# Performance work log

Hardware: AMD Instinct MI355X
Metric: run time of the kernel (lower is better)

## Reference

```python
import jax, jax.numpy as jnp
import numpy as np
from jax import lax

B, T_MEL, M = 4, 63, 80
HOP, K_UP, WIN = 256, 800, 1024
R, S, Q = 120, 240, 256
NB, K, CYCLE = 16, 2, 8
PAD_UP = (K_UP + 4 * HOP - WIN) // 2  # 400
L = (T_MEL - 1) * HOP  # 15872


def conv1d(x, w, b, dilation=1, pad=(0, 0)):
    # x: [B,Cin,L], w: [Cout,Cin,K]
    y = lax.conv_general_dilated(x, w, (1,), [pad], rhs_dilation=(dilation,),
                                 dimension_numbers=('NCH', 'OIH', 'NCH'))
    return y + b[None, :, None]


def setup_inputs() -> dict:
    key = jax.random.key(0)
    ks = jax.random.split(key, 20)
    rn = lambda k, shape, s=0.05: (jax.random.normal(k, shape, jnp.float32) * s)
    return {
        'waveforms': jax.random.normal(ks[0], (B, L), jnp.float32),
        'melspecs': jax.random.normal(ks[1], (B, M, T_MEL), jnp.float32),
        # ConvTranspose1d weight, torch layout (in, out, k)
        'w_up': rn(ks[2], (M, M, K_UP)), 'b_up': rn(ks[3], (M,)),
        'w_in': rn(ks[4], (R, 1, 1)), 'b_in': rn(ks[5], (R,)),
        # per-block params stacked on leading axis
        'w_gate': rn(ks[6], (NB, 2 * R, R, K)), 'b_gate': rn(ks[7], (NB, 2 * R)),
        'w_cond': rn(ks[8], (NB, 2 * R, M, 1)), 'b_cond': rn(ks[9], (NB, 2 * R)),
        'w_res': rn(ks[10], (NB, R, R, 1)), 'b_res': rn(ks[11], (NB, R)),
        'w_skip': rn(ks[12], (NB, S, R, 1)), 'b_skip': rn(ks[13], (NB, S)),
        'w_h1': rn(ks[14], (Q, S, 1)), 'b_h1': rn(ks[15], (Q,)),
        'w_h2': rn(ks[16], (Q, Q, 1)), 'b_h2': rn(ks[17], (Q,)),
    }


def reference(waveforms, melspecs, w_up, b_up, w_in, b_in, w_gate, b_gate,
              w_cond, b_cond, w_res, b_res, w_skip, b_skip, w_h1, b_h1, w_h2, b_h2):
    # upsample = ConvTranspose1d: lhs-dilated conv with flipped, transposed kernel
    wt = jnp.flip(jnp.transpose(w_up, (1, 0, 2)), -1)  # [out,in,k]
    p = K_UP - 1 - PAD_UP  # 399
    conditions = lax.conv_general_dilated(
        melspecs, wt, (1,), [(p, p)], lhs_dilation=(HOP,),
        dimension_numbers=('NCH', 'OIH', 'NCH')) + b_up[None, :, None]

    length = min(waveforms.shape[-1], conditions.shape[-1])
    wav = waveforms[..., :length]
    cond = conditions[..., :length]

    residuals = conv1d(wav[:, None, :], w_in, b_in)  # [B,R,L]
    skips = jnp.zeros((wav.shape[0], S, length), residuals.dtype)
    for i in range(NB):
        d = 2 ** (i % CYCLE)
        gated = conv1d(residuals, w_gate[i], b_gate[i], dilation=d, pad=((K - 1) * d, 0))
        gated = gated + conv1d(cond, w_cond[i], b_cond[i])
        f, g = jnp.split(gated, 2, axis=1)
        z = jnp.tanh(f) * jax.nn.sigmoid(g)  # [B,R,L]
        skips = skips + conv1d(z, w_skip[i], b_skip[i])
        residuals = residuals + conv1d(z, w_res[i], b_res[i])

    h = conv1d(jax.nn.relu(skips), w_h1, b_h1)
    logits = conv1d(jax.nn.relu(h), w_h2, b_h2)  # [B,Q,L]
    return logits
```

## Files before the change

kernel.cpp:

```cpp
#include <hip/hip_runtime.h>
#include <math.h>

#define B_   4
#define M_   80
#define TMEL 63
#define R_   120
#define S_   240
#define Q_   256
#define NB_  16
#define L_   15872

typedef float  f32x4  __attribute__((ext_vector_type(4)));
typedef short  bf16x8 __attribute__((ext_vector_type(8)));
typedef short  short4_t __attribute__((ext_vector_type(4)));

__device__ __forceinline__ short f2bf(float x) {
  unsigned u = __builtin_bit_cast(unsigned, x);
  u += 0x7fffu + ((u >> 16) & 1u);
  return (short)(u >> 16);
}
__device__ __forceinline__ float bf2f(unsigned short s) {
  unsigned u = ((unsigned)s) << 16;
  return __builtin_bit_cast(float, u);
}

__global__ __launch_bounds__(256) void prep_melT_kernel(
    const float* __restrict__ mel, short* __restrict__ melT)
{
  const int idx = blockIdx.x * 256 + threadIdx.x;
  if (idx >= B_ * TMEL * M_) return;
  const int m = idx % M_;
  const int i = (idx / M_) % TMEL;
  const int b = idx / (M_ * TMEL);
  melT[idx] = f2bf(mel[b * (M_ * TMEL) + m * TMEL + i]);
}

__global__ __launch_bounds__(256) void prep_wup_kernel(
    const float* __restrict__ w_up, short* __restrict__ Wup)
{
  __shared__ float T[M_][65];
  const int c  = blockIdx.x >> 4;
  const int j  = (blockIdx.x >> 2) & 3;
  const int fb = blockIdx.x & 3;
  for (int idx = threadIdx.x; idx < M_ * 64; idx += 256) {
    const int pl = idx & 63, m = idx >> 6;
    const int phi = fb * 64 + pl;
    const int dmin = (phi < 112) ? -1 : -2;
    const int dmax = (phi < 144) ? 1 : 0;
    const int delta = dmin + j;
    float v = 0.0f;
    if (delta <= dmax)
      v = w_up[m * (M_ * 800) + c * 800 + (400 + phi + 256 * delta)];
    T[m][pl] = v;
  }
  __syncthreads();
  for (int idx = threadIdx.x; idx < 64 * M_; idx += 256) {
    const int m = idx % M_, pl = idx / M_;
    const int phi = fb * 64 + pl;
    Wup[((size_t)phi * M_ + c) * 320 + j * 80 + m] = f2bf(T[m][pl]);
  }
}

#define KPU 328

__global__ __launch_bounds__(256, 2) void upsample_mfma_kernel(
    const short* __restrict__ melT, const short* __restrict__ Wup,
    const float* __restrict__ b_up, short* __restrict__ condb)
{
  __shared__ __align__(16) short Xu[64 * KPU];
  const int tid = threadIdx.x;
  const int phi = blockIdx.x;
  const int r0 = blockIdx.y * 64;
  const int dmin = (phi < 112) ? -1 : -2;

  for (int idx = tid; idx < 2560; idx += 256) {
    const int v = idx % 10;
    const int j = (idx / 10) & 3;
    const int rl = idx / 40;
    const int rho = r0 + rl;
    const int b = rho / 62;
    const int n = rho - b * 62;
    const int i = n - (dmin + j);
    int4 val = make_int4(0, 0, 0, 0);
    if (b < B_ && i >= 0 && i < TMEL)
      val = *(const int4*)&melT[((size_t)b * TMEL + i) * M_ + v * 8];
    *(int4*)&Xu[rl * KPU + j * 80 + v * 8] = val;
  }
  __syncthreads();

  const int lane = tid & 63;
  const int wv = tid >> 6;
  const int col = lane & 15;
  const int quad = lane >> 4;
  const int kq = quad * 8;

  f32x4 acc[5];
#pragma unroll
  for (int i = 0; i < 5; ++i) acc[i] = (f32x4)(0.f);
#pragma unroll
  for (int ks = 0; ks < 10; ++ks) {
    bf16x8 a = *(const bf16x8*)&Xu[(wv * 16 + col) * KPU + ks * 32 + kq];
#pragma unroll
    for (int ct = 0; ct < 5; ++ct) {
      bf16x8 b = *(const bf16x8*)(Wup + ((size_t)phi * M_ + ct * 16 + col) * 320 + ks * 32 + kq);
      acc[ct] = __builtin_amdgcn_mfma_f32_16x16x32_bf16(a, b, acc[ct], 0, 0, 0);
    }
  }
#pragma unroll
  for (int ct = 0; ct < 5; ++ct) {
    const int c = ct * 16 + col;
    const float bc = b_up[c];
#pragma unroll
    for (int reg = 0; reg < 4; ++reg) {
      const int rho = r0 + wv * 16 + quad * 4 + reg;
      if (rho < 248) {
        const int b = rho / 62;
        const int n = rho - b * 62;
        const int t = phi + (n << 8);
        condb[((size_t)b * L_ + t) * M_ + c] = f2bf(acc[ct][reg] + bc);
      }
    }
  }
}

__global__ __launch_bounds__(256) void in_conv_kernel(
    const float* __restrict__ wav, const float* __restrict__ w_in,
    const float* __restrict__ b_in, float* __restrict__ res)
{
  const int idx = blockIdx.x * 256 + threadIdx.x;
  const int r = idx & 127;
  const int rem = idx >> 7;
  const int t = rem % L_;
  const int b = rem / L_;
  res[idx] = (r < R_) ? (w_in[r] * wav[b * L_ + t] + b_in[r]) : 0.0f;
}

__global__ __launch_bounds__(256) void prepack_w1_kernel(
    const float* __restrict__ wg, const float* __restrict__ wc,
    short* __restrict__ W1p)
{
  const int idx = blockIdx.x * 256 + threadIdx.x;
  const int k = idx % 320;
  const int cp = (idx / 320) % 256;
  const int i = idx / (320 * 256);
  float val = 0.0f;
  if (cp < 240) {
    const int r = cp >> 1;
    const int corig = (cp & 1) ? (120 + r) : r;
    if (k < 120)      val = wg[((size_t)(i * 240 + corig) * 120 + k) * 2 + 0];
    else if (k < 240) val = wg[((size_t)(i * 240 + corig) * 120 + (k - 120)) * 2 + 1];
    else              val = wc[(size_t)(i * 240 + corig) * 80 + (k - 240)];
  }
  W1p[idx] = f2bf(val);
}

__global__ __launch_bounds__(256) void prepack_w2_kernel(
    const float* __restrict__ wsk, const float* __restrict__ wr,
    short* __restrict__ W2p)
{
  const int idx = blockIdx.x * 256 + threadIdx.x;
  const int k = idx % 128;
  const int sp = (idx / 128) % 384;
  const int i = idx / (128 * 384);
  float val = 0.0f;
  if (k < 120) {
    if (sp < 240)      val = wsk[(size_t)(i * 240 + sp) * 120 + k];
    else if (sp < 360) val = wr[(size_t)(i * 120 + (sp - 240)) * 120 + k];
  }
  W2p[idx] = f2bf(val);
}

__global__ __launch_bounds__(256) void prepack_rest_kernel(
    const float* __restrict__ wh1, const float* __restrict__ wh2,
    const float* __restrict__ bg, const float* __restrict__ bc,
    const float* __restrict__ bs, const float* __restrict__ br,
    short* __restrict__ Wh1p, short* __restrict__ Wh2p,
    float* __restrict__ bias1p, float* __restrict__ bias2p)
{
  const int idx = blockIdx.x * 256 + threadIdx.x;
  if (idx < 65536) {
    const int q = idx >> 8, k = idx & 255;
    Wh1p[idx] = f2bf(k < 240 ? wh1[q * 240 + k] : 0.0f);
  } else if (idx < 131072) {
    Wh2p[idx - 65536] = f2bf(wh2[idx - 65536]);
  } else if (idx < 134912) {
    const int j = idx - 131072;
    const int i = j / 240, cp = j % 240;
    const int r = cp >> 1;
    const int corig = (cp & 1) ? (120 + r) : r;
    bias1p[j] = bg[i * 240 + corig] + bc[i * 240 + corig];
  } else if (idx < 141056) {
    const int j = idx - 134912;
    const int i = j / 384, sp = j % 384;
    float v = 0.0f;
    if (sp < 240)      v = bs[i * 240 + sp];
    else if (sp < 360) v = br[i * 120 + (sp - 240)];
    bias2p[j] = v;
  }
}

#define KP1 320
#define KP2 136
#define SGP 248
#define NTILE (L_ / 64)
#define NWG   (NTILE * B_)
#define CPX   (NWG / 8)

__device__ __forceinline__ int xswz(int row, int k) {
  return row * KP1 + (k ^ ((row & 7) << 3));
}

__global__ __launch_bounds__(512, 4) void block_mfma_kernel(
    const float* __restrict__ res_in, float* __restrict__ res_out,
    unsigned short* __restrict__ skips, const short* __restrict__ condb,
    const short* __restrict__ W1, const short* __restrict__ W2,
    const float* __restrict__ bias1, const float* __restrict__ bias2,
    const int d, const int first)
{
  __shared__ __align__(16) short Xs[64 * KP1];
  short* const Zs = Xs;

  const int tid = threadIdx.x;
  const int w_id = blockIdx.y * NTILE + blockIdx.x;
  const int nid  = (w_id & 7) * CPX + (w_id >> 3);
  const int bb   = nid / NTILE;
  const int t0   = (nid - bb * NTILE) * 64;

  {
    const int dd = (d <= 64) ? d : 64;
    const int nr = 64 + dd;
    for (int idx = tid; idx < nr * 30; idx += 512) {
      const int rr = idx / 30, c4 = idx - rr * 30;
      int ts;
      if (d <= 64)      ts = t0 - d + rr;
      else              ts = (rr < 64) ? (t0 - 128 + rr) : (t0 + rr - 64);
      float4 v = make_float4(0.f, 0.f, 0.f, 0.f);
      if (ts >= 0)
        v = *(const float4*)(res_in + ((size_t)(bb * L_ + ts) * 128 + c4 * 4));
      short4_t s;
      s.x = f2bf(v.x); s.y = f2bf(v.y); s.z = f2bf(v.z); s.w = f2bf(v.w);
      if (rr < 64)
        *(short4_t*)&Xs[xswz(rr, c4 * 4)] = s;
      const int r1 = rr - dd;
      if (r1 >= 0)
        *(short4_t*)&Xs[xswz(r1, 120 + c4 * 4)] = s;
    }
  }
  for (int idx = tid; idx < 640; idx += 512) {
    const int c = idx % 10, trw = idx / 10;
    const int4 v = *(const int4*)(condb + ((size_t)(bb * L_ + t0 + trw) * M_ + c * 8));
    *(int4*)&Xs[xswz(trw, 240 + c * 8)] = v;
  }
  __syncthreads();

  const int lane = tid & 63;
  const int wv = tid >> 6;
  const int col = lane & 15;
  const int quad = lane >> 4;
  const int kq = quad * 8;

  f32x4 acc[4][2];
#pragma unroll
  for (int a = 0; a < 4; ++a)
#pragma unroll
    for (int b = 0; b < 2; ++b) acc[a][b] = (f32x4)(0.f);
#pragma unroll
  for (int ks = 0; ks < 10; ++ks) {
    bf16x8 av[4];
#pragma unroll
    for (int tf = 0; tf < 4; ++tf)
      av[tf] = *(const bf16x8*)&Xs[xswz(tf * 16 + col, ks * 32 + kq)];
#pragma unroll
    for (int ct = 0; ct < 2; ++ct) {
      bf16x8 b = *(const bf16x8*)(W1 + ((wv * 2 + ct) * 16 + col) * 320 + ks * 32 + kq);
#pragma unroll
      for (int tf = 0; tf < 4; ++tf)
        acc[tf][ct] = __builtin_amdgcn_mfma_f32_16x16x32_bf16(av[tf], b, acc[tf][ct], 0, 0, 0);
    }
  }

  __syncthreads();

#pragma unroll
  for (int ct = 0; ct < 2; ++ct) {
    const int tile = wv * 2 + ct;
    if (tile < 15) {
      const int cp = tile * 16 + col;
      const float bias = bias1[cp];
#pragma unroll
      for (int tf = 0; tf < 4; ++tf) {
#pragma unroll
        for (int reg = 0; reg < 4; ++reg) {
          float v = acc[tf][ct][reg] + bias;
          v = fminf(fmaxf(v, -15.f), 15.f);
          const float e = __expf((lane & 1) ? -v : 2.0f * v);
          const float rc = __builtin_amdgcn_rcpf(e + 1.0f);
          const float u = (lane & 1) ? rc : (e - 1.0f) * rc;
          const float p = __shfl_xor(u, 1, 64);
          if (!(lane & 1)) {
            const int t = tf * 16 + quad * 4 + reg;
            Zs[t * KP2 + tile * 8 + (col >> 1)] = f2bf(u * p);
          }
        }
      }
    }
  }
  if (tid < 64)
    *(int4*)&Zs[tid * KP2 + 120] = make_int4(0, 0, 0, 0);
  __syncthreads();

  f32x4 acc2[4][3];
#pragma unroll
  for (int a = 0; a < 4; ++a)
#pragma unroll
    for (int b = 0; b < 3; ++b) acc2[a][b] = (f32x4)(0.f);
#pragma unroll
  for (int ks = 0; ks < 4; ++ks) {
    bf16x8 av[4];
#pragma unroll
    for (int tf = 0; tf < 4; ++tf)
      av[tf] = *(const bf16x8*)&Zs[(tf * 16 + col) * KP2 + ks * 32 + kq];
#pragma unroll
    for (int st = 0; st < 3; ++st) {
      bf16x8 b = *(const bf16x8*)(W2 + ((wv * 3 + st) * 16 + col) * 128 + ks * 32 + kq);
#pragma unroll
      for (int tf = 0; tf < 4; ++tf)
        acc2[tf][st] = __builtin_amdgcn_mfma_f32_16x16x32_bf16(av[tf], b, acc2[tf][st], 0, 0, 0);
    }
  }

  __syncthreads();

  short* SG = Xs;
#pragma unroll
  for (int st = 0; st < 3; ++st) {
    const int tile = wv * 3 + st;
    if (tile < 15) {
      const int s = tile * 16 + col;
      const float b2 = bias2[s];
#pragma unroll
      for (int tf = 0; tf < 4; ++tf)
#pragma unroll
        for (int reg = 0; reg < 4; ++reg)
          SG[(tf * 16 + quad * 4 + reg) * SGP + s] = f2bf(acc2[tf][st][reg] + b2);
    } else if (tile < 23) {
      const int s = tile * 16 + col;
      const int r = s - 240;
      if (r < 120) {
        const float b2 = bias2[s];
#pragma unroll
        for (int tf = 0; tf < 4; ++tf) {
#pragma unroll
          for (int reg = 0; reg < 4; ++reg) {
            const int t = tf * 16 + quad * 4 + reg;
            const size_t gi = ((size_t)(bb * L_ + t0 + t)) * 128 + r;
            res_out[gi] = res_in[gi] + acc2[tf][st][reg] + b2;
          }
        }
      }
    }
  }
  __syncthreads();

  {
    const size_t srow = ((size_t)bb * L_ + t0) * 240;
#pragma unroll
    for (int it = 0; it < 4; ++it) {
      const int idx = tid + it * 512;
      if (idx < 1920) {
        const int row = idx / 30;
        const int j = idx - row * 30;
        unsigned short* gp = skips + srow + row * 240 + j * 8;
        int4 sv = *(const int4*)&SG[row * SGP + j * 8];
        const unsigned short* svp = (const unsigned short*)&sv;
        float vals[8];
#pragma unroll
        for (int e = 0; e < 8; ++e) vals[e] = bf2f(svp[e]);
        if (!first) {
          int4 ov = *(const int4*)gp;
          const unsigned short* ovp = (const unsigned short*)&ov;
#pragma unroll
          for (int e = 0; e < 8; ++e) vals[e] += bf2f(ovp[e]);
        }
        int4 res;
        unsigned short* rp = (unsigned short*)&res;
#pragma unroll
        for (int e = 0; e < 8; ++e) rp[e] = (unsigned short)f2bf(vals[e]);
        *(int4*)gp = res;
      }
    }
  }
}

#define KPH 264

__global__ __launch_bounds__(256, 2) void head_mfma_kernel(
    const unsigned short* __restrict__ skips,
    const short* __restrict__ Wh1, const short* __restrict__ Wh2,
    const float* __restrict__ bh1, const float* __restrict__ bh2,
    float* __restrict__ out)
{
  __shared__ __align__(16) short Ss[64 * KPH];
  short* const Hs = Ss;

  const int tid = threadIdx.x;
  const int w_id = blockIdx.y * NTILE + blockIdx.x;
  const int nid  = (w_id & 7) * CPX + (w_id >> 3);
  const int bb   = nid / NTILE;
  const int t0   = (nid - bb * NTILE) * 64;

  for (int idx = tid; idx < 2048; idx += 256) {
    const int c = idx & 31, trw = idx >> 5;
    if (c < 30) {
      int4 v = *(const int4*)(skips + ((size_t)(bb * L_ + t0 + trw) * 240 + c * 8));
      int* vi = (int*)&v;
#pragma unroll
      for (int j = 0; j < 4; ++j) {
        unsigned x = (unsigned)vi[j];
        unsigned lo = x & 0xFFFFu; if (lo & 0x8000u) lo = 0;
        unsigned hi = x >> 16;     if (hi & 0x8000u) hi = 0;
        vi[j] = (int)(lo | (hi << 16));
      }
      *(int4*)&Ss[trw * KPH + c * 8] = v;
    } else {
      *(int4*)&Ss[trw * KPH + c * 8] = make_int4(0, 0, 0, 0);
    }
  }
  __syncthreads();

  const int lane = tid & 63;
  const int wv = tid >> 6;
  const int col = lane & 15;
  const int quad = lane >> 4;
  const int kq = quad * 8;

  f32x4 acc[4][4];
#pragma unroll
  for (int a = 0; a < 4; ++a)
#pragma unroll
    for (int b = 0; b < 4; ++b) acc[a][b] = (f32x4)(0.f);
#pragma unroll
  for (int ks = 0; ks < 8; ++ks) {
    bf16x8 av[4];
#pragma unroll
    for (int tf = 0; tf < 4; ++tf)
      av[tf] = *(const bf16x8*)&Ss[(tf * 16 + col) * KPH + ks * 32 + kq];
#pragma unroll
    for (int ct = 0; ct < 4; ++ct) {
      bf16x8 b = *(const bf16x8*)(Wh1 + ((wv * 4 + ct) * 16 + col) * 256 + ks * 32 + kq);
#pragma unroll
      for (int tf = 0; tf < 4; ++tf)
        acc[tf][ct] = __builtin_amdgcn_mfma_f32_16x16x32_bf16(av[tf], b, acc[tf][ct], 0, 0, 0);
    }
  }

  __syncthreads();

#pragma unroll
  for (int ct = 0; ct < 4; ++ct) {
    const int q = (wv * 4 + ct) * 16 + col;
    const float b1 = bh1[q];
#pragma unroll
    for (int tf = 0; tf < 4; ++tf)
#pragma unroll
      for (int reg = 0; reg < 4; ++reg)
        Hs[(tf * 16 + quad * 4 + reg) * KPH + q] = f2bf(fmaxf(acc[tf][ct][reg] + b1, 0.0f));
  }
  __syncthreads();

  f32x4 acc2[4][4];
#pragma unroll
  for (int a = 0; a < 4; ++a)
#pragma unroll
    for (int b = 0; b < 4; ++b) acc2[a][b] = (f32x4)(0.f);
#pragma unroll
  for (int ks = 0; ks < 8; ++ks) {
    bf16x8 av[4];
#pragma unroll
    for (int tf = 0; tf < 4; ++tf)
      av[tf] = *(const bf16x8*)&Hs[(tf * 16 + col) * KPH + ks * 32 + kq];
#pragma unroll
    for (int ct = 0; ct < 4; ++ct) {
      bf16x8 b = *(const bf16x8*)(Wh2 + ((wv * 4 + ct) * 16 + col) * 256 + ks * 32 + kq);
#pragma unroll
      for (int tf = 0; tf < 4; ++tf)
        acc2[tf][ct] = __builtin_amdgcn_mfma_f32_16x16x32_bf16(av[tf], b, acc2[tf][ct], 0, 0, 0);
    }
  }
#pragma unroll
  for (int ct = 0; ct < 4; ++ct) {
    const int q = (wv * 4 + ct) * 16 + col;
    const float b2 = bh2[q];
#pragma unroll
    for (int tf = 0; tf < 4; ++tf) {
      const int tg0 = t0 + tf * 16 + quad * 4;
      float4 o = make_float4(acc2[tf][ct][0] + b2, acc2[tf][ct][1] + b2,
                             acc2[tf][ct][2] + b2, acc2[tf][ct][3] + b2);
      *(float4*)(out + ((size_t)(bb * Q_ + q)) * L_ + tg0) = o;
    }
  }
}

extern "C" void kernel_launch(void* const* d_in, const int* in_sizes, int n_in,
                              void* d_out, int out_size, void* d_ws, size_t ws_size,
                              hipStream_t stream) {
  const float* wav    = (const float*)d_in[0];
  const float* mel    = (const float*)d_in[1];
  const float* w_up   = (const float*)d_in[2];
  const float* b_up   = (const float*)d_in[3];
  const float* w_in   = (const float*)d_in[4];
  const float* b_in   = (const float*)d_in[5];
  const float* w_gate = (const float*)d_in[6];
  const float* b_gate = (const float*)d_in[7];
  const float* w_cond = (const float*)d_in[8];
  const float* b_cond = (const float*)d_in[9];
  const float* w_res  = (const float*)d_in[10];
  const float* b_res  = (const float*)d_in[11];
  const float* w_skip = (const float*)d_in[12];
  const float* b_skip = (const float*)d_in[13];
  const float* w_h1   = (const float*)d_in[14];
  const float* b_h1   = (const float*)d_in[15];
  const float* w_h2   = (const float*)d_in[16];
  const float* b_h2   = (const float*)d_in[17];
  float* out = (float*)d_out;

  char* w = (char*)d_ws;
  short* condb   = (short*)w;                 w += (size_t)B_ * L_ * M_ * 2;
  float* res0    = (float*)w;                 w += (size_t)B_ * L_ * 128 * 4;
  float* res1    = (float*)w;                 w += (size_t)B_ * L_ * 128 * 4;
  unsigned short* skips = (unsigned short*)w; w += (size_t)B_ * L_ * 240 * 2;
  short* W1p     = (short*)w;                 w += (size_t)16 * 256 * 320 * 2;
  short* W2p     = (short*)w;                 w += (size_t)16 * 384 * 128 * 2;
  short* Wh1p    = (short*)w;                 w += (size_t)256 * 256 * 2;
  short* Wh2p    = (short*)w;                 w += (size_t)256 * 256 * 2;
  float* bias1p  = (float*)w;                 w += (size_t)16 * 240 * 4;
  float* bias2p  = (float*)w;                 w += (size_t)16 * 384 * 4;
  short* melT    = (short*)w;                 w += (size_t)B_ * TMEL * M_ * 2;
  short* Wup = (short*)skips;

  prepack_w1_kernel<<<(16 * 256 * 320) / 256, 256, 0, stream>>>(w_gate, w_cond, W1p);
  prepack_w2_kernel<<<(16 * 384 * 128) / 256, 256, 0, stream>>>(w_skip, w_res, W2p);
  prepack_rest_kernel<<<141056 / 256, 256, 0, stream>>>(
      w_h1, w_h2, b_gate, b_cond, b_skip, b_res, Wh1p, Wh2p, bias1p, bias2p);
  prep_melT_kernel<<<(B_ * TMEL * M_ + 255) / 256, 256, 0, stream>>>(mel, melT);
  prep_wup_kernel<<<80 * 4 * 4, 256, 0, stream>>>(w_up, Wup);

  dim3 ugrid(256, 4);
  upsample_mfma_kernel<<<ugrid, 256, 0, stream>>>(melT, Wup, b_up, condb);
  in_conv_kernel<<<((size_t)B_ * L_ * 128) / 256, 256, 0, stream>>>(wav, w_in, b_in, res0);

  dim3 bgrid(L_ / 64, B_);
  for (int i = 0; i < NB_; ++i) {
    const int d = 1 << (i & 7);
    const float* rin  = (i & 1) ? res1 : res0;
    float*       rout = (i & 1) ? res0 : res1;
    block_mfma_kernel<<<bgrid, 512, 0, stream>>>(
        rin, rout, skips, condb,
        W1p + (size_t)i * 256 * 320, W2p + (size_t)i * 384 * 128,
        bias1p + i * 240, bias2p + i * 384,
        d, (i == 0) ? 1 : 0);
  }

  head_mfma_kernel<<<bgrid, 256, 0, stream>>>(skips, Wh1p, Wh2p, b_h1, b_h2, out);
}
```

Before: 1.123 ms.

## Store residual stream in bf16, prefetch skip accumulators, and raise MFMA wave priority

```diff
diff --git a/kernel.cpp b/kernel.cpp
--- a/kernel.cpp
+++ b/kernel.cpp
@@ -125,14 +125,14 @@
 
 __global__ __launch_bounds__(256) void in_conv_kernel(
     const float* __restrict__ wav, const float* __restrict__ w_in,
-    const float* __restrict__ b_in, float* __restrict__ res)
+    const float* __restrict__ b_in, short* __restrict__ res)
 {
   const int idx = blockIdx.x * 256 + threadIdx.x;
   const int r = idx & 127;
   const int rem = idx >> 7;
   const int t = rem % L_;
   const int b = rem / L_;
-  res[idx] = (r < R_) ? (w_in[r] * wav[b * L_ + t] + b_in[r]) : 0.0f;
+  res[idx] = (r < R_) ? f2bf(w_in[r] * wav[b * L_ + t] + b_in[r]) : (short)0;
 }
 
 __global__ __launch_bounds__(256) void prepack_w1_kernel(
@@ -211,7 +211,7 @@
 }
 
 __global__ __launch_bounds__(512, 4) void block_mfma_kernel(
-    const float* __restrict__ res_in, float* __restrict__ res_out,
+    const short* __restrict__ res_in, short* __restrict__ res_out,
     unsigned short* __restrict__ skips, const short* __restrict__ condb,
     const short* __restrict__ W1, const short* __restrict__ W2,
     const float* __restrict__ bias1, const float* __restrict__ bias2,
@@ -229,21 +229,19 @@
   {
     const int dd = (d <= 64) ? d : 64;
     const int nr = 64 + dd;
-    for (int idx = tid; idx < nr * 30; idx += 512) {
-      const int rr = idx / 30, c4 = idx - rr * 30;
+    for (int idx = tid; idx < nr * 15; idx += 512) {
+      const int rr = idx / 15, c8 = idx - rr * 15;
       int ts;
       if (d <= 64)      ts = t0 - d + rr;
       else              ts = (rr < 64) ? (t0 - 128 + rr) : (t0 + rr - 64);
-      float4 v = make_float4(0.f, 0.f, 0.f, 0.f);
+      int4 v = make_int4(0, 0, 0, 0);
       if (ts >= 0)
-        v = *(const float4*)(res_in + ((size_t)(bb * L_ + ts) * 128 + c4 * 4));
-      short4_t s;
-      s.x = f2bf(v.x); s.y = f2bf(v.y); s.z = f2bf(v.z); s.w = f2bf(v.w);
+        v = *(const int4*)(res_in + ((size_t)(bb * L_ + ts) * 128 + c8 * 8));
       if (rr < 64)
-        *(short4_t*)&Xs[xswz(rr, c4 * 4)] = s;
+        *(int4*)&Xs[xswz(rr, c8 * 8)] = v;
       const int r1 = rr - dd;
       if (r1 >= 0)
-        *(short4_t*)&Xs[xswz(r1, 120 + c4 * 4)] = s;
+        *(int4*)&Xs[xswz(r1, 120 + c8 * 8)] = v;
     }
   }
   for (int idx = tid; idx < 640; idx += 512) {
@@ -264,6 +262,7 @@
   for (int a = 0; a < 4; ++a)
 #pragma unroll
     for (int b = 0; b < 2; ++b) acc[a][b] = (f32x4)(0.f);
+  __builtin_amdgcn_s_setprio(1);
 #pragma unroll
   for (int ks = 0; ks < 10; ++ks) {
     bf16x8 av[4];
@@ -278,6 +277,7 @@
         acc[tf][ct] = __builtin_amdgcn_mfma_f32_16x16x32_bf16(av[tf], b, acc[tf][ct], 0, 0, 0);
     }
   }
+  __builtin_amdgcn_s_setprio(0);
 
   __syncthreads();
 
@@ -309,11 +309,37 @@
     *(int4*)&Zs[tid * KP2 + 120] = make_int4(0, 0, 0, 0);
   __syncthreads();
 
+  const size_t srow = ((size_t)bb * L_ + t0) * 240;
+  int4 sk0 = make_int4(0,0,0,0), sk1 = sk0, sk2 = sk0, sk3 = sk0;
+  if (!first) {
+    {
+      const int idx = tid;
+      const int row = idx / 30, j = idx - row * 30;
+      sk0 = *(const int4*)(skips + srow + row * 240 + j * 8);
+    }
+    {
+      const int idx = tid + 512;
+      const int row = idx / 30, j = idx - row * 30;
+      sk1 = *(const int4*)(skips + srow + row * 240 + j * 8);
+    }
+    {
+      const int idx = tid + 1024;
+      const int row = idx / 30, j = idx - row * 30;
+      sk2 = *(const int4*)(skips + srow + row * 240 + j * 8);
+    }
+    if (tid + 1536 < 1920) {
+      const int idx = tid + 1536;
+      const int row = idx / 30, j = idx - row * 30;
+      sk3 = *(const int4*)(skips + srow + row * 240 + j * 8);
+    }
+  }
+
   f32x4 acc2[4][3];
 #pragma unroll
   for (int a = 0; a < 4; ++a)
 #pragma unroll
     for (int b = 0; b < 3; ++b) acc2[a][b] = (f32x4)(0.f);
+  __builtin_amdgcn_s_setprio(1);
 #pragma unroll
   for (int ks = 0; ks < 4; ++ks) {
     bf16x8 av[4];
@@ -328,6 +354,7 @@
         acc2[tf][st] = __builtin_amdgcn_mfma_f32_16x16x32_bf16(av[tf], b, acc2[tf][st], 0, 0, 0);
     }
   }
+  __builtin_amdgcn_s_setprio(0);
 
   __syncthreads();
 
@@ -354,7 +381,7 @@
           for (int reg = 0; reg < 4; ++reg) {
             const int t = tf * 16 + quad * 4 + reg;
             const size_t gi = ((size_t)(bb * L_ + t0 + t)) * 128 + r;
-            res_out[gi] = res_in[gi] + acc2[tf][st][reg] + b2;
+            res_out[gi] = f2bf(bf2f((unsigned short)res_in[gi]) + acc2[tf][st][reg] + b2);
           }
         }
       }
@@ -363,7 +390,6 @@
   __syncthreads();
 
   {
-    const size_t srow = ((size_t)bb * L_ + t0) * 240;
 #pragma unroll
     for (int it = 0; it < 4; ++it) {
       const int idx = tid + it * 512;
@@ -377,7 +403,7 @@
 #pragma unroll
         for (int e = 0; e < 8; ++e) vals[e] = bf2f(svp[e]);
         if (!first) {
-          int4 ov = *(const int4*)gp;
+          const int4 ov = (it == 0) ? sk0 : (it == 1) ? sk1 : (it == 2) ? sk2 : sk3;
           const unsigned short* ovp = (const unsigned short*)&ov;
 #pragma unroll
           for (int e = 0; e < 8; ++e) vals[e] += bf2f(ovp[e]);
@@ -526,8 +552,8 @@
 
   char* w = (char*)d_ws;
   short* condb   = (short*)w;                 w += (size_t)B_ * L_ * M_ * 2;
-  float* res0    = (float*)w;                 w += (size_t)B_ * L_ * 128 * 4;
-  float* res1    = (float*)w;                 w += (size_t)B_ * L_ * 128 * 4;
+  short* res0    = (short*)w;                 w += (size_t)B_ * L_ * 128 * 2;
+  short* res1    = (short*)w;                 w += (size_t)B_ * L_ * 128 * 2;
   unsigned short* skips = (unsigned short*)w; w += (size_t)B_ * L_ * 240 * 2;
   short* W1p     = (short*)w;                 w += (size_t)16 * 256 * 320 * 2;
   short* W2p     = (short*)w;                 w += (size_t)16 * 384 * 128 * 2;
@@ -552,8 +578,8 @@
   dim3 bgrid(L_ / 64, B_);
   for (int i = 0; i < NB_; ++i) {
     const int d = 1 << (i & 7);
-    const float* rin  = (i & 1) ? res1 : res0;
-    float*       rout = (i & 1) ? res0 : res1;
+    const short* rin  = (i & 1) ? res1 : res0;
+    short*       rout = (i & 1) ? res0 : res1;
     block_mfma_kernel<<<bgrid, 512, 0, stream>>>(
         rin, rout, skips, condb,
         W1p + (size_t)i * 256 * 320, W2p + (size_t)i * 384 * 128,
```

After: 1.080 ms. 3.9% less time.
